# Kernel tuning notes

Hardware: AMD Instinct MI355X
Metric: run time of the kernel (lower is better)

Reference implementation:

```python
import jax, jax.numpy as jnp
import numpy as np

EPS = 1e-12  # torch F.normalize clamp_min eps


def masked_softmax(inputs, mask):
    # faithful to the torch helper: stable-shift, exp, mask, guard zero-sum
    inputs = inputs - jnp.max(inputs, axis=-1, keepdims=True)
    exp = jnp.exp(inputs) * mask
    sum_exp = jnp.sum(exp, axis=-1, keepdims=True)
    return exp / jnp.where(sum_exp == 0, jnp.ones_like(sum_exp), sum_exp)


def setup_inputs() -> dict:
    key = jax.random.key(0)
    kx, km, kw, kb, ku, kuo = jax.random.split(key, 6)
    B, S, D, A, O = 128, 1024, 256, 256, 256  # output_dim must equal input_dim
    x = jax.random.normal(kx, (B, S, D), dtype=jnp.float32)
    mask = jax.random.randint(km, (B, S), 0, 2).astype(jnp.float32)
    w_omega = jax.random.normal(kw, (D, A), dtype=jnp.float32) * 0.05
    b_omega = jax.random.normal(kb, (A,), dtype=jnp.float32) * 0.05
    u_omega = jax.random.normal(ku, (A,), dtype=jnp.float32) * 0.05
    u_omega_o = jax.random.normal(kuo, (A, O), dtype=jnp.float32) * 0.05
    return {"x": x, "mask": mask, "w_omega": w_omega, "b_omega": b_omega,
            "u_omega": u_omega, "u_omega_o": u_omega_o}


def reference(x, mask, w_omega, b_omega, u_omega, u_omega_o):
    # t = L2-normalize(x @ W + b) along last dim (F.normalize with eps clamp)
    t = jnp.einsum('bsd,da->bsa', x, w_omega) + b_omega
    t = t / jnp.maximum(jnp.linalg.norm(t, axis=-1, keepdims=True), EPS)
    v = jnp.tanh(t)                                   # [B,S,A]
    vu = jnp.einsum('bsa,a->bs', v, u_omega)          # [B,S]
    vu_o = jnp.einsum('bsa,ao->bso', v, u_omega_o)    # [B,S,O]
    vu = vu * mask
    mask_o = mask[..., None]                          # [B,S,1]
    vu_o = vu_o * mask_o
    alphas = masked_softmax(vu, mask)                 # softmax over S
    betas = masked_softmax(vu_o, mask_o)              # softmax over O
    w = alphas[..., None] * betas                     # [B,S,O]
    output = jnp.sum(x * w, axis=-2)                  # [B,O] (O == D)
    return output, alphas, betas
```

## Files before the change

### kernel.cpp

```cpp
#include <hip/hip_runtime.h>
#include <math.h>

#define B_ 128
#define S_ 1024
#define D_ 256
#define XP 264
#define TP 68
#define ROWS 32

using bf16x8 = __attribute__((ext_vector_type(8))) __bf16;
using bf16x4 = __attribute__((ext_vector_type(4))) __bf16;
using f32x4  = __attribute__((ext_vector_type(4))) float;

__device__ __forceinline__ float qred_add(float v) {
    v += __shfl_xor(v, 1); v += __shfl_xor(v, 2);
    v += __shfl_xor(v, 4); v += __shfl_xor(v, 8);
    return v;
}
__device__ __forceinline__ float wred_add(float x) {
#pragma unroll
    for (int off = 32; off > 0; off >>= 1) x += __shfl_xor(x, off, 64);
    return x;
}

__global__ __launch_bounds__(256) void k_prep(
    const float* __restrict__ W, const float* __restrict__ Uo,
    __bf16* __restrict__ Wf, __bf16* __restrict__ Uf)
{
    const int e = blockIdx.x * 256 + threadIdx.x;
    const int frag = e >> 9, rem = e & 511;
    const int lane = rem >> 3, j = rem & 7;
    const int kk = frag >> 4, tn = frag & 15;
    const int k = kk * 32 + (lane >> 4) * 8 + j;
    const int n = tn * 16 + (lane & 15);
    Wf[e] = (__bf16)W[k * 256 + n];
    Uf[e] = (__bf16)Uo[k * 256 + n];
}

__global__ __launch_bounds__(256, 3) void k_rows(
    const float* __restrict__ x, const float* __restrict__ mask,
    const __bf16* __restrict__ Wf, const float* __restrict__ bo,
    const float* __restrict__ u, const __bf16* __restrict__ Uf,
    float* __restrict__ e_out,
    float* __restrict__ betas,
    float* __restrict__ part,
    float* __restrict__ outraw,
    const int use_part)
{
    __shared__ __align__(16) char smem[4 * 16 * TP * 4];
    __bf16* xs   = (__bf16*)smem;
    float* trans = (float*)smem;
    __shared__ float red[4][ROWS];
    __shared__ float red2[4][ROWS];
    const int tid = threadIdx.x, lane = tid & 63, w = tid >> 6;
    const int quad = lane >> 4, c = lane & 15;
    const int hi = lane >> 4, c4 = lane & 15;
    const int row0 = blockIdx.x * ROWS;
    const bf16x8* Wf8 = (const bf16x8*)Wf;
    const bf16x8* Uf8 = (const bf16x8*)Uf;

    {
        const float4* xg = (const float4*)(x + (size_t)row0 * D_);
#pragma unroll
        for (int it = 0; it < 8; ++it) {
            const int r = it * 4 + w;
            const float4 t = xg[r * 64 + lane];
            bf16x4 h; h[0] = (__bf16)t.x; h[1] = (__bf16)t.y; h[2] = (__bf16)t.z; h[3] = (__bf16)t.w;
            *(bf16x4*)(xs + r * XP + lane * 4) = h;
        }
    }

    __syncthreads();

    f32x4 acc[2][4];
#pragma unroll
    for (int i = 0; i < 2; ++i)
#pragma unroll
        for (int j = 0; j < 4; ++j) acc[i][j] = (f32x4){0.f, 0.f, 0.f, 0.f};
#pragma unroll
    for (int kk = 0; kk < 8; ++kk) {
        bf16x8 a[2], b[4];
#pragma unroll
        for (int i = 0; i < 2; ++i)
            a[i] = *(const bf16x8*)(xs + (i * 16 + c) * XP + kk * 32 + quad * 8);
#pragma unroll
        for (int j = 0; j < 4; ++j)
            b[j] = Wf8[(kk * 16 + w * 4 + j) * 64 + lane];
#pragma unroll
        for (int i = 0; i < 2; ++i)
#pragma unroll
            for (int j = 0; j < 4; ++j)
                acc[i][j] = __builtin_amdgcn_mfma_f32_16x16x32_bf16(a[i], b[j], acc[i][j], 0, 0, 0);
    }

#pragma unroll
    for (int j = 0; j < 4; ++j) {
        const float bj = bo[w * 64 + j * 16 + c];
#pragma unroll
        for (int i = 0; i < 2; ++i)
#pragma unroll
            for (int r = 0; r < 4; ++r) acc[i][j][r] += bj;
    }
    {
        float myv = 0.f;
#pragma unroll
        for (int i = 0; i < 2; ++i)
#pragma unroll
            for (int r = 0; r < 4; ++r) {
                float s = 0.f;
#pragma unroll
                for (int j = 0; j < 4; ++j) s += acc[i][j][r] * acc[i][j][r];
                const float p = qred_add(s);
                if (c == i * 4 + r) myv = p;
            }
        if (c < 8) red[w][(c >> 2) * 16 + quad * 4 + (c & 3)] = myv;
    }
    __syncthreads();

    float inv[2][4];
#pragma unroll
    for (int i = 0; i < 2; ++i)
#pragma unroll
        for (int r = 0; r < 4; ++r) {
            const int row = i * 16 + quad * 4 + r;
            const float t = red[0][row] + red[1][row] + red[2][row] + red[3][row];
            inv[i][r] = 1.f / fmaxf(sqrtf(t), 1e-12f);
        }

    float uj[4];
#pragma unroll
    for (int j = 0; j < 4; ++j) uj[j] = u[w * 64 + j * 16 + c];
    float vup[2][4];
#pragma unroll
    for (int i = 0; i < 2; ++i)
#pragma unroll
        for (int r = 0; r < 4; ++r) vup[i][r] = 0.f;
#pragma unroll
    for (int i = 0; i < 2; ++i)
#pragma unroll
        for (int j = 0; j < 4; ++j)
#pragma unroll
            for (int r = 0; r < 4; ++r) {
                const float tv = acc[i][j][r] * inv[i][r];
                const float e2 = __expf(2.f * tv);
                const float v  = (e2 - 1.f) * __frcp_rn(e2 + 1.f);
                vup[i][r] += v * uj[j];
                xs[(i * 16 + quad * 4 + r) * XP + (w * 64 + j * 16 + c)] = (__bf16)v;
            }
    {
        float myv = 0.f;
#pragma unroll
        for (int i = 0; i < 2; ++i)
#pragma unroll
            for (int r = 0; r < 4; ++r) {
                const float p = qred_add(vup[i][r]);
                if (c == i * 4 + r) myv = p;
            }
        if (c < 8) red2[w][(c >> 2) * 16 + quad * 4 + (c & 3)] = myv;
    }
    __syncthreads();

    float ev[2][4];
#pragma unroll
    for (int i = 0; i < 2; ++i)
#pragma unroll
        for (int p = 0; p < 4; ++p) {
            const int rr = i * 16 + hi + p * 4;
            const float vu = red2[0][rr] + red2[1][rr] + red2[2][rr] + red2[3][rr];
            ev[i][p] = __expf(vu) * mask[row0 + rr];
        }
    if (tid < ROWS) {
        const float vu = red2[0][tid] + red2[1][tid] + red2[2][tid] + red2[3][tid];
        e_out[row0 + tid] = __expf(vu) * mask[row0 + tid];
    }

#pragma unroll
    for (int i = 0; i < 2; ++i)
#pragma unroll
        for (int j = 0; j < 4; ++j) acc[i][j] = (f32x4){0.f, 0.f, 0.f, 0.f};
#pragma unroll
    for (int kk = 0; kk < 8; ++kk) {
        bf16x8 a[2], b[4];
#pragma unroll
        for (int i = 0; i < 2; ++i)
            a[i] = *(const bf16x8*)(xs + (i * 16 + c) * XP + kk * 32 + quad * 8);
#pragma unroll
        for (int j = 0; j < 4; ++j)
            b[j] = Uf8[(kk * 16 + w * 4 + j) * 64 + lane];
#pragma unroll
        for (int i = 0; i < 2; ++i)
#pragma unroll
            for (int j = 0; j < 4; ++j)
                acc[i][j] = __builtin_amdgcn_mfma_f32_16x16x32_bf16(a[i], b[j], acc[i][j], 0, 0, 0);
    }

    float mk[2][4];
#pragma unroll
    for (int i = 0; i < 2; ++i)
#pragma unroll
        for (int r = 0; r < 4; ++r) mk[i][r] = mask[row0 + i * 16 + quad * 4 + r];
#pragma unroll
    for (int i = 0; i < 2; ++i)
#pragma unroll
        for (int j = 0; j < 4; ++j)
#pragma unroll
            for (int r = 0; r < 4; ++r) {
                const float t = acc[i][j][r] * mk[i][r];
                acc[i][j][r] = __expf(t) * mk[i][r];
            }
    {
        float myv = 0.f;
#pragma unroll
        for (int i = 0; i < 2; ++i)
#pragma unroll
            for (int r = 0; r < 4; ++r) {
                float s = 0.f;
#pragma unroll
                for (int j = 0; j < 4; ++j) s += acc[i][j][r];
                const float p = qred_add(s);
                if (c == i * 4 + r) myv = p;
            }
        if (c < 8) red[w][(c >> 2) * 16 + quad * 4 + (c & 3)] = myv;
    }
    __syncthreads();

    float rs[2][4];
#pragma unroll
    for (int i = 0; i < 2; ++i)
#pragma unroll
        for (int p = 0; p < 4; ++p) {
            const int rr = i * 16 + hi + p * 4;
            const float s = red[0][rr] + red[1][rr] + red[2][rr] + red[3][rr];
            rs[i][p] = 1.f / ((s == 0.f) ? 1.f : s);
        }

    float* tw = trans + w * (16 * TP);
    f32x4 opart = (f32x4){0.f, 0.f, 0.f, 0.f};
#pragma unroll
    for (int i = 0; i < 2; ++i) {
        asm volatile("s_waitcnt lgkmcnt(0)" ::: "memory");
#pragma unroll
        for (int j = 0; j < 4; ++j)
#pragma unroll
            for (int r = 0; r < 4; ++r)
                tw[(quad * 4 + r) * TP + j * 16 + c] = acc[i][j][r];
        asm volatile("s_waitcnt lgkmcnt(0)" ::: "memory");
#pragma unroll
        for (int p = 0; p < 4; ++p) {
            const int rl = hi + p * 4;
            f32x4 b4 = *(const f32x4*)&tw[rl * TP + c4 * 4];
            const float rsv = rs[i][p];
            b4[0] *= rsv; b4[1] *= rsv; b4[2] *= rsv; b4[3] *= rsv;
            const size_t goff = (size_t)(row0 + i * 16 + rl) * D_ + w * 64 + c4 * 4;
            __builtin_nontemporal_store(b4, (f32x4*)&betas[goff]);
            const float evv = ev[i][p];
            if (evv != 0.f) {
                const f32x4 x4 = *(const f32x4*)&x[goff];
                opart[0] += evv * b4[0] * x4[0];
                opart[1] += evv * b4[1] * x4[1];
                opart[2] += evv * b4[2] * x4[2];
                opart[3] += evv * b4[3] * x4[3];
            }
        }
    }
#pragma unroll
    for (int k = 0; k < 4; ++k) {
        opart[k] += __shfl_xor(opart[k], 16);
        opart[k] += __shfl_xor(opart[k], 32);
    }
    if (lane < 16) {
        const int col = w * 64 + c4 * 4;
        if (use_part) {
            *(f32x4*)&part[(size_t)blockIdx.x * D_ + col] = opart;
        } else {
            const int b = row0 >> 10;
#pragma unroll
            for (int k = 0; k < 4; ++k) atomicAdd(&outraw[b * D_ + col + k], opart[k]);
        }
    }
}

__global__ __launch_bounds__(256) void k_fin(
    const float* __restrict__ part, float* __restrict__ e_alphas,
    float* __restrict__ out, const int use_part)
{
    const int b = blockIdx.x;
    const int tid = threadIdx.x, lane = tid & 63, wid = tid >> 6;
    __shared__ float red[4];
    const int base = b * S_;
    float ev[4];
#pragma unroll
    for (int k = 0; k < 4; ++k) ev[k] = e_alphas[base + tid + 256 * k];
    float s = ev[0] + ev[1] + ev[2] + ev[3];
    s = wred_add(s);
    if (lane == 0) red[wid] = s;
    __syncthreads();
    const float Z = red[0] + red[1] + red[2] + red[3];
    const float Zr = 1.f / ((Z == 0.f) ? 1.f : Z);
#pragma unroll
    for (int k = 0; k < 4; ++k) e_alphas[base + tid + 256 * k] = ev[k] * Zr;

    float acc;
    if (use_part) {
        acc = 0.f;
#pragma unroll
        for (int k = 0; k < 32; ++k) acc += part[(size_t)(b * 32 + k) * D_ + tid];
    } else {
        acc = out[b * D_ + tid];
    }
    out[b * D_ + tid] = acc * Zr;
}

extern "C" void kernel_launch(void* const* d_in, const int* in_sizes, int n_in,
                              void* d_out, int out_size, void* d_ws, size_t ws_size,
                              hipStream_t stream) {
    const float* x    = (const float*)d_in[0];
    const float* mask = (const float*)d_in[1];
    const float* W    = (const float*)d_in[2];
    const float* bo   = (const float*)d_in[3];
    const float* u    = (const float*)d_in[4];
    const float* Uo   = (const float*)d_in[5];

    float* out    = (float*)d_out;
    float* alphas = out + B_ * D_;
    float* betas  = alphas + (size_t)B_ * S_;

    __bf16* Wf = (__bf16*)d_ws;
    __bf16* Uf = Wf + 65536;
    float* part = (float*)(Uf + 65536);

    const int nblk = B_ * S_ / ROWS;
    const size_t need = 2 * 65536 * sizeof(__bf16) + (size_t)nblk * D_ * sizeof(float);
    const int use_part = (ws_size >= need) ? 1 : 0;

    if (!use_part)
        hipMemsetAsync(out, 0, (size_t)B_ * D_ * sizeof(float), stream);
    k_prep<<<256, 256, 0, stream>>>(W, Uo, Wf, Uf);
    k_rows<<<nblk, 256, 0, stream>>>(x, mask, Wf, bo, u, Uf, alphas, betas, part, out, use_part);
    k_fin <<<B_,   256, 0, stream>>>(part, alphas, out, use_part);
}
```

Measured before the change: 104.6 us.

## Split fused row kernel into two kernels passing tanh activations via betas buffer

```diff
diff --git a/kernel.cpp b/kernel.cpp
--- a/kernel.cpp
+++ b/kernel.cpp
@@ -37,27 +37,21 @@
     Uf[e] = (__bf16)Uo[k * 256 + n];
 }
 
-__global__ __launch_bounds__(256, 3) void k_rows(
+__global__ __launch_bounds__(256, 4) void k_g1(
     const float* __restrict__ x, const float* __restrict__ mask,
     const __bf16* __restrict__ Wf, const float* __restrict__ bo,
-    const float* __restrict__ u, const __bf16* __restrict__ Uf,
+    const float* __restrict__ u,
     float* __restrict__ e_out,
-    float* __restrict__ betas,
-    float* __restrict__ part,
-    float* __restrict__ outraw,
-    const int use_part)
+    float* __restrict__ vscr)
 {
-    __shared__ __align__(16) char smem[4 * 16 * TP * 4];
-    __bf16* xs   = (__bf16*)smem;
-    float* trans = (float*)smem;
+    __shared__ __align__(16) char smem[ROWS * XP * 2];
+    __bf16* xs = (__bf16*)smem;
     __shared__ float red[4][ROWS];
     __shared__ float red2[4][ROWS];
     const int tid = threadIdx.x, lane = tid & 63, w = tid >> 6;
     const int quad = lane >> 4, c = lane & 15;
-    const int hi = lane >> 4, c4 = lane & 15;
     const int row0 = blockIdx.x * ROWS;
     const bf16x8* Wf8 = (const bf16x8*)Wf;
-    const bf16x8* Uf8 = (const bf16x8*)Uf;
 
     {
         const float4* xg = (const float4*)(x + (size_t)row0 * D_);
@@ -69,7 +63,6 @@
             *(bf16x4*)(xs + r * XP + lane * 4) = h;
         }
     }
-
     __syncthreads();
 
     f32x4 acc[2][4];
@@ -160,20 +153,40 @@
     }
     __syncthreads();
 
-    float ev[2][4];
-#pragma unroll
-    for (int i = 0; i < 2; ++i)
-#pragma unroll
-        for (int p = 0; p < 4; ++p) {
-            const int rr = i * 16 + hi + p * 4;
-            const float vu = red2[0][rr] + red2[1][rr] + red2[2][rr] + red2[3][rr];
-            ev[i][p] = __expf(vu) * mask[row0 + rr];
-        }
     if (tid < ROWS) {
         const float vu = red2[0][tid] + red2[1][tid] + red2[2][tid] + red2[3][tid];
         e_out[row0 + tid] = __expf(vu) * mask[row0 + tid];
     }
 
+    bf16x8* vf8 = (bf16x8*)(vscr + (size_t)blockIdx.x * (ROWS * D_));
+    const int kkb = 2 * w;
+#pragma unroll
+    for (int kk2 = 0; kk2 < 2; ++kk2)
+#pragma unroll
+        for (int i = 0; i < 2; ++i) {
+            const bf16x8 av = *(const bf16x8*)(xs + (i * 16 + c) * XP + (kkb + kk2) * 32 + quad * 8);
+            vf8[((kkb + kk2) * 2 + i) * 64 + lane] = av;
+        }
+}
+
+__global__ __launch_bounds__(256, 4) void k_g2(
+    const float* __restrict__ x, const float* __restrict__ mask,
+    const __bf16* __restrict__ Uf, const float* __restrict__ e_out,
+    float* betas,
+    float* __restrict__ part,
+    float* __restrict__ outraw,
+    const int use_part)
+{
+    __shared__ __align__(16) float trans[4][16 * TP];
+    __shared__ float red[4][ROWS];
+    const int tid = threadIdx.x, lane = tid & 63, w = tid >> 6;
+    const int quad = lane >> 4, c = lane & 15;
+    const int hi = lane >> 4, c4 = lane & 15;
+    const int row0 = blockIdx.x * ROWS;
+    const bf16x8* Uf8 = (const bf16x8*)Uf;
+    const bf16x8* vf8 = (const bf16x8*)(betas + (size_t)blockIdx.x * (ROWS * D_));
+
+    f32x4 acc[2][4];
 #pragma unroll
     for (int i = 0; i < 2; ++i)
 #pragma unroll
@@ -183,7 +196,7 @@
         bf16x8 a[2], b[4];
 #pragma unroll
         for (int i = 0; i < 2; ++i)
-            a[i] = *(const bf16x8*)(xs + (i * 16 + c) * XP + kk * 32 + quad * 8);
+            a[i] = vf8[(kk * 2 + i) * 64 + lane];
 #pragma unroll
         for (int j = 0; j < 4; ++j)
             b[j] = Uf8[(kk * 16 + w * 4 + j) * 64 + lane];
@@ -194,20 +207,15 @@
                 acc[i][j] = __builtin_amdgcn_mfma_f32_16x16x32_bf16(a[i], b[j], acc[i][j], 0, 0, 0);
     }
 
-    float mk[2][4];
-#pragma unroll
-    for (int i = 0; i < 2; ++i)
-#pragma unroll
-        for (int r = 0; r < 4; ++r) mk[i][r] = mask[row0 + i * 16 + quad * 4 + r];
-#pragma unroll
-    for (int i = 0; i < 2; ++i)
-#pragma unroll
-        for (int j = 0; j < 4; ++j)
-#pragma unroll
-            for (int r = 0; r < 4; ++r) {
-                const float t = acc[i][j][r] * mk[i][r];
-                acc[i][j][r] = __expf(t) * mk[i][r];
-            }
+#pragma unroll
+    for (int i = 0; i < 2; ++i)
+#pragma unroll
+        for (int r = 0; r < 4; ++r) {
+            const float m = mask[row0 + i * 16 + quad * 4 + r];
+#pragma unroll
+            for (int j = 0; j < 4; ++j)
+                acc[i][j][r] = __expf(acc[i][j][r] * m) * m;
+        }
     {
         float myv = 0.f;
 #pragma unroll
@@ -224,17 +232,18 @@
     }
     __syncthreads();
 
-    float rs[2][4];
+    float ev[2][4], rs[2][4];
 #pragma unroll
     for (int i = 0; i < 2; ++i)
 #pragma unroll
         for (int p = 0; p < 4; ++p) {
             const int rr = i * 16 + hi + p * 4;
+            ev[i][p] = e_out[row0 + rr];
             const float s = red[0][rr] + red[1][rr] + red[2][rr] + red[3][rr];
             rs[i][p] = 1.f / ((s == 0.f) ? 1.f : s);
         }
 
-    float* tw = trans + w * (16 * TP);
+    float* tw = trans[w];
     f32x4 opart = (f32x4){0.f, 0.f, 0.f, 0.f};
 #pragma unroll
     for (int i = 0; i < 2; ++i) {
@@ -336,6 +345,7 @@
     if (!use_part)
         hipMemsetAsync(out, 0, (size_t)B_ * D_ * sizeof(float), stream);
     k_prep<<<256, 256, 0, stream>>>(W, Uo, Wf, Uf);
-    k_rows<<<nblk, 256, 0, stream>>>(x, mask, Wf, bo, u, Uf, alphas, betas, part, out, use_part);
-    k_fin <<<B_,   256, 0, stream>>>(part, alphas, out, use_part);
-}
+    k_g1 <<<nblk, 256, 0, stream>>>(x, mask, Wf, bo, u, alphas, betas);
+    k_g2 <<<nblk, 256, 0, stream>>>(x, mask, Uf, alphas, betas, part, out, use_part);
+    k_fin<<<B_,   256, 0, stream>>>(part, alphas, out, use_part);
+}
```

Measured after the change: 112.0 us. 1.07x slower.
